# Performance work log

Measured on AMD Instinct MI355X. Metric: run time of the kernel, lower is better.

The kernel has to match this reference:

```python
import jax, jax.numpy as jnp
import numpy as np

IMG_SIZE = 640
STRIDES = (8, 16, 32)
KA = 3          # anchors per level
C = 80          # num classes
CONF_THRESH = 0.001
NMS_THRESH = 0.6
TOPK = 4096     # fixed candidate cap for jit-compatible NMS


def setup_inputs() -> dict:
    key = jax.random.key(0)
    k1, k2, k3 = jax.random.split(key, 3)
    ch = KA * (1 + C + 4)  # 255
    pred_s = jax.random.normal(k1, (ch, 80, 80), dtype=jnp.float32)
    pred_m = jax.random.normal(k2, (ch, 40, 40), dtype=jnp.float32)
    pred_l = jax.random.normal(k3, (ch, 20, 20), dtype=jnp.float32)
    # classic YOLOv3 anchors, [level, anchor, (w,h)]
    anchor_size = jnp.array(
        [[[10, 13], [16, 30], [33, 23]],
         [[30, 61], [62, 45], [59, 119]],
         [[116, 90], [156, 198], [373, 326]]], dtype=jnp.float32)
    return {"pred_s": pred_s, "pred_m": pred_m, "pred_l": pred_l,
            "anchor_size": anchor_size}


def _decode_level(pred, anchors, stride):
    # pred: [KA*(1+C+4), H, W]; anchors: [KA, 2]
    H, W = pred.shape[1], pred.shape[2]
    p = jnp.transpose(pred, (1, 2, 0))                    # [H, W, ch]
    obj = p[..., :KA].reshape(-1, 1)                      # [H*W*KA, 1]
    cls = p[..., KA:KA * (1 + C)].reshape(-1, C)          # [H*W*KA, C]
    reg = p[..., KA * (1 + C):].reshape(H * W, KA, 4)     # [H*W, KA, 4]
    gy, gx = jnp.meshgrid(jnp.arange(H), jnp.arange(W), indexing="ij")
    grid = jnp.stack([gx, gy], -1).reshape(-1, 1, 2).astype(pred.dtype)  # [H*W,1,2]
    # center_sample = False branch
    xy = (jax.nn.sigmoid(reg[..., :2]) + grid) * stride
    wh = jnp.exp(reg[..., 2:]) * anchors[None, :, :]
    box = jnp.concatenate([xy - 0.5 * wh, xy + 0.5 * wh], -1).reshape(-1, 4)
    return obj, cls, box


def _decode(pred_s, pred_m, pred_l, anchor_size):
    parts = [_decode_level(p, anchor_size[i], STRIDES[i])
             for i, p in enumerate([pred_s, pred_m, pred_l])]
    obj = jnp.concatenate([p[0] for p in parts], 0)       # [N,1]
    cls = jnp.concatenate([p[1] for p in parts], 0)       # [N,C]
    box = jnp.concatenate([p[2] for p in parts], 0)       # [N,4]
    bboxes = jnp.clip(box / IMG_SIZE, 0.0, 1.0)
    scores = jax.nn.sigmoid(obj) * jax.nn.softmax(cls, axis=-1)
    return bboxes, scores


def reference(pred_s, pred_m, pred_l, anchor_size):
    bboxes, scores = _decode(pred_s, pred_m, pred_l, anchor_size)
    cls_inds = jnp.argmax(scores, axis=1)                 # [N]
    sc = jnp.max(scores, axis=1)                          # [N]
    sc_masked = jnp.where(sc >= CONF_THRESH, sc, -1.0)
    top_sc, idx = jax.lax.top_k(sc_masked, TOPK)          # candidates, score-sorted
    b = bboxes[idx]                                       # [K,4]
    c = cls_inds[idx]                                     # [K]
    valid = top_sc >= CONF_THRESH                         # [K]
    # pairwise IoU, exactly as the numpy NMS computes it
    x1, y1, x2, y2 = b[:, 0], b[:, 1], b[:, 2], b[:, 3]
    area = (x2 - x1) * (y2 - y1)
    xx1 = jnp.maximum(x1[:, None], x1[None, :])
    yy1 = jnp.maximum(y1[:, None], y1[None, :])
    xx2 = jnp.minimum(x2[:, None], x2[None, :])
    yy2 = jnp.minimum(y2[:, None], y2[None, :])
    w = jnp.maximum(1e-28, xx2 - xx1)
    h = jnp.maximum(1e-28, yy2 - yy1)
    inter = w * h
    iou = inter / (area[:, None] + area[None, :] - inter + 1e-14)
    # sup[j, i] = kept j (earlier in score order) suppresses i, same class only
    order = jnp.arange(TOPK)
    sup = (c[:, None] == c[None, :]) & (iou > NMS_THRESH) \
          & (order[:, None] < order[None, :])
    def body(i, keep):
        ki = valid[i] & ~jnp.any(keep & sup[:, i])
        return keep.at[i].set(ki)
    keep = jax.lax.fori_loop(0, TOPK, body, jnp.zeros(TOPK, dtype=bool))
    return b, top_sc, c, keep
```

## Files before the change

kernel.cpp:

```cpp
#include <hip/hip_runtime.h>
#include <cstdint>
#include <cstddef>

#define N_ANCH 25200
#define NB0 19200
#define NB1 24000
#define TOPK_N 4096
#define CONF_T 0.001
#define NMS_T 0.6
#define IMGS 640.0
#define NBINS 16384
#define JS 16

typedef unsigned long long u64;

struct WS {
  double sc[N_ANCH];
  double box[N_ANCH][4];
  int    cls[N_ANCH];
  int    rank[N_ANCH];
  int    subset[N_ANCH];
  int    hist[NBINS];
  int    m_count;
  int    t_bin;
  double tbox[TOPK_N][4];
  double tarea[TOPK_N];
  double tsc[TOPK_N];
  int    tcls[TOPK_N];
  u64    supT[TOPK_N * 64];
  u64    hasSup[64];
};

__device__ __forceinline__ double dsigmoid(double x) { return 1.0 / (1.0 + exp(-x)); }

__device__ __forceinline__ int score_bin(double sc) {
  if (sc < 0.0) return 0;
  return (int)(__float_as_uint((float)sc) >> 16);
}

__global__ void k_zero(WS* __restrict__ ws) {
  int t = blockIdx.x * 256 + threadIdx.x;
  ws->hist[t] = 0;
  if (t < 64) ws->hasSup[t] = 0ull;
  if (t == 64) ws->m_count = 0;
  if (t == 65) ws->t_bin = 0;
}

__global__ void k_decode(const float* __restrict__ ps, const float* __restrict__ pm,
                         const float* __restrict__ pl, const float* __restrict__ anch,
                         WS* __restrict__ ws) {
  int a = blockIdx.x * 256 + threadIdx.x;
  if (a >= N_ANCH) return;
  const float* p; int W, base, lvl; double stride;
  if (a < NB0)      { p = ps; W = 80; base = 0;   lvl = 0; stride = 8.0; }
  else if (a < NB1) { p = pm; W = 40; base = NB0; lvl = 1; stride = 16.0; }
  else              { p = pl; W = 20; base = NB1; lvl = 2; stride = 32.0; }
  int e = a - base;
  int pos = e / 3;
  int k = e - 3 * pos;
  int HW = W * W;
  int x = pos % W, y = pos / W;

  double sobj = dsigmoid((double)p[(size_t)k * HW + pos]);

  const float* pc = p + (size_t)(3 + k * 80) * HW + pos;
  double m = -1e300, ssum = 0.0; int am = 0;
  for (int c = 0; c < 80; ++c) {
    double v = (double)pc[(size_t)c * HW];
    ssum += exp(v);
    if (v > m) { m = v; am = c; }
  }
  double sc = sobj * (exp(m) / ssum);

  const float* pr = p + (size_t)(243 + k * 4) * HW + pos;
  double tx = (double)pr[0];
  double ty = (double)pr[(size_t)HW];
  double tw = (double)pr[(size_t)2 * HW];
  double th = (double)pr[(size_t)3 * HW];
  double cx = (dsigmoid(tx) + (double)x) * stride;
  double cy = (dsigmoid(ty) + (double)y) * stride;
  double aw = (double)anch[lvl * 6 + k * 2 + 0];
  double ah = (double)anch[lvl * 6 + k * 2 + 1];
  double bw = exp(tw) * aw;
  double bh = exp(th) * ah;
  double x1 = fmin(fmax((cx - 0.5 * bw) / IMGS, 0.0), 1.0);
  double y1 = fmin(fmax((cy - 0.5 * bh) / IMGS, 0.0), 1.0);
  double x2 = fmin(fmax((cx + 0.5 * bw) / IMGS, 0.0), 1.0);
  double y2 = fmin(fmax((cy + 0.5 * bh) / IMGS, 0.0), 1.0);

  ws->box[a][0] = x1; ws->box[a][1] = y1;
  ws->box[a][2] = x2; ws->box[a][3] = y2;
  ws->cls[a] = am;
  double scm = (sc >= CONF_T) ? sc : -1.0;
  ws->sc[a] = scm;
  atomicAdd(&ws->hist[score_bin(scm)], 1);
}

__global__ void k_select(WS* __restrict__ ws) {
  __shared__ int part[256];
  int t = threadIdx.x;
  const int CH = NBINS / 256;
  int sum = 0;
  for (int r = 0; r < CH; ++r) sum += ws->hist[NBINS - 1 - (t * CH + r)];
  part[t] = sum;
  __syncthreads();
  for (int off = 1; off < 256; off <<= 1) {
    int v = (t >= off) ? part[t - off] : 0;
    __syncthreads();
    part[t] += v;
    __syncthreads();
  }
  int exc = part[t] - sum;
  int cum = exc;
  for (int r = 0; r < CH; ++r) {
    int b = NBINS - 1 - (t * CH + r);
    int h = ws->hist[b];
    int prev = cum;
    cum += h;
    if (prev < TOPK_N && cum >= TOPK_N) ws->t_bin = b;
  }
}

__global__ void k_compact(WS* __restrict__ ws) {
  int i = blockIdx.x * 256 + threadIdx.x;
  if (i >= N_ANCH) return;
  int tb = ws->t_bin;
  if (score_bin(ws->sc[i]) >= tb) {
    int idx = atomicAdd(&ws->m_count, 1);
    ws->subset[idx] = i;
    ws->rank[idx] = 0;
  }
}

__global__ void k_rank(WS* __restrict__ ws) {
  const int CHUNK = 1024;
  __shared__ double sj[CHUNK];
  __shared__ int    aj[CHUNK];
  int m = ws->m_count;
  if ((int)blockIdx.x * 256 >= m) return;
  int i = blockIdx.x * 256 + threadIdx.x;
  bool active = (i < m);
  int ai = active ? ws->subset[i] : 0;
  double si = active ? ws->sc[ai] : -2.0;

  int jlen = (m + JS - 1) / JS;
  int j0 = blockIdx.y * jlen;
  int jend = min(j0 + jlen, m);
  int cnt = 0;
  for (int jc = j0; jc < jend; jc += CHUNK) {
    int n = min(CHUNK, jend - jc);
    __syncthreads();
    for (int t = threadIdx.x; t < n; t += 256) {
      int a = ws->subset[jc + t];
      aj[t] = a;
      sj[t] = ws->sc[a];
    }
    __syncthreads();
    if (active) {
      for (int t = 0; t < n; ++t) {
        double s = sj[t];
        cnt += (int)((s > si) | ((s == si) & (aj[t] < ai)));
      }
    }
  }
  if (active && cnt) atomicAdd(&ws->rank[i], cnt);
}

__global__ void k_scatter(WS* __restrict__ ws, float* __restrict__ out) {
  int m = ws->m_count;
  int i = blockIdx.x * 256 + threadIdx.x;
  if (i >= m) return;
  int r = ws->rank[i];
  if (r >= TOPK_N) return;
  int a = ws->subset[i];
  double b0 = ws->box[a][0], b1 = ws->box[a][1];
  double b2 = ws->box[a][2], b3 = ws->box[a][3];
  double s  = ws->sc[a];
  int    c  = ws->cls[a];
  ws->tbox[r][0] = b0; ws->tbox[r][1] = b1;
  ws->tbox[r][2] = b2; ws->tbox[r][3] = b3;
  ws->tarea[r] = (b2 - b0) * (b3 - b1);
  ws->tsc[r] = s;
  ws->tcls[r] = c;
  out[r * 4 + 0] = (float)b0;
  out[r * 4 + 1] = (float)b1;
  out[r * 4 + 2] = (float)b2;
  out[r * 4 + 3] = (float)b3;
  out[4 * TOPK_N + r] = (float)s;
  out[5 * TOPK_N + r] = (float)c;
}

__global__ void k_iou(WS* __restrict__ ws) {
  __shared__ double jb[64][5];
  __shared__ int jc[64];
  int tid = threadIdx.x;
  int w = blockIdx.y;
  if (tid < 64) {
    int j = w * 64 + tid;
    jb[tid][0] = ws->tbox[j][0];
    jb[tid][1] = ws->tbox[j][1];
    jb[tid][2] = ws->tbox[j][2];
    jb[tid][3] = ws->tbox[j][3];
    jb[tid][4] = ws->tarea[j];
    jc[tid] = ws->tcls[j];
  }
  __syncthreads();
  int i = blockIdx.x * 256 + tid;
  double x1 = ws->tbox[i][0], y1 = ws->tbox[i][1];
  double x2 = ws->tbox[i][2], y2 = ws->tbox[i][3];
  double ai = ws->tarea[i];
  int ci = ws->tcls[i];
  u64 bits = 0;
  int jbase = w * 64;
  for (int t = 0; t < 64; ++t) {
    double xx1 = fmax(x1, jb[t][0]);
    double yy1 = fmax(y1, jb[t][1]);
    double xx2 = fmin(x2, jb[t][2]);
    double yy2 = fmin(y2, jb[t][3]);
    double iw = fmax(1e-28, xx2 - xx1);
    double ih = fmax(1e-28, yy2 - yy1);
    double inter = iw * ih;
    double denom = ai + jb[t][4] - inter + 1e-14;
    bool sup = (jc[t] == ci) && (inter > NMS_T * denom) && ((jbase + t) < i);
    bits |= ((u64)sup) << t;
  }
  ws->supT[(size_t)i * 64 + w] = bits;
  if (bits) atomicOr(&ws->hasSup[i >> 6], 1ull << (i & 63));
}

__global__ void __launch_bounds__(64) k_nms(const WS* __restrict__ ws, float* __restrict__ out) {
  __shared__ u64 hsArr[64];
  __shared__ int lst[TOPK_N];
  int lane = threadIdx.x;

  u64 validw = 0;
  for (int b = 0; b < 64; ++b)
    validw |= ((u64)(ws->tsc[lane * 64 + b] >= CONF_T)) << b;

  u64 hasw = ws->hasSup[lane];
  u64 keepw = validw & ~hasw;
  hsArr[lane] = hasw;
  __syncthreads();

  int K = 0;
  for (int l = 0; l < 64; ++l) {
    u64 w = hsArr[l];
    while (w) {
      int b = __builtin_ctzll(w);
      w &= w - 1;
      if (lane == 0) lst[K] = l * 64 + b;
      ++K;
    }
  }
  __syncthreads();

  const u64* ST = ws->supT;
  int IA[16], IB[16];
  u64 A[16], B[16];

#pragma unroll
  for (int r = 0; r < 16; ++r) IA[r] = (r < K) ? lst[r] : 0;
#pragma unroll
  for (int r = 0; r < 16; ++r) A[r] = (r < K) ? ST[(size_t)IA[r] * 64 + lane] : 0ull;

  for (int base = 0; base < K; base += 32) {
#pragma unroll
    for (int r = 0; r < 16; ++r) IB[r] = (base + 16 + r < K) ? lst[base + 16 + r] : 0;
#pragma unroll
    for (int r = 0; r < 16; ++r) B[r] = (base + 16 + r < K) ? ST[(size_t)IB[r] * 64 + lane] : 0ull;
#pragma unroll
    for (int r = 0; r < 16; ++r) {
      if (base + r < K) {
        int i = IA[r];
        u64 bal = __ballot((keepw & A[r]) != 0ull);
        if (lane == (i >> 6) && bal == 0ull && ((validw >> (i & 63)) & 1ull))
          keepw |= 1ull << (i & 63);
      }
    }
#pragma unroll
    for (int r = 0; r < 16; ++r) IA[r] = (base + 32 + r < K) ? lst[base + 32 + r] : 0;
#pragma unroll
    for (int r = 0; r < 16; ++r) A[r] = (base + 32 + r < K) ? ST[(size_t)IA[r] * 64 + lane] : 0ull;
#pragma unroll
    for (int r = 0; r < 16; ++r) {
      if (base + 16 + r < K) {
        int i = IB[r];
        u64 bal = __ballot((keepw & B[r]) != 0ull);
        if (lane == (i >> 6) && bal == 0ull && ((validw >> (i & 63)) & 1ull))
          keepw |= 1ull << (i & 63);
      }
    }
  }

  for (int b = 0; b < 64; ++b)
    out[6 * TOPK_N + lane * 64 + b] = (float)((keepw >> b) & 1ull);
}

extern "C" void kernel_launch(void* const* d_in, const int* in_sizes, int n_in,
                              void* d_out, int out_size, void* d_ws, size_t ws_size,
                              hipStream_t stream) {
  const float* ps   = (const float*)d_in[0];
  const float* pm   = (const float*)d_in[1];
  const float* pl   = (const float*)d_in[2];
  const float* anch = (const float*)d_in[3];
  float* out = (float*)d_out;
  WS* ws = (WS*)d_ws;

  dim3 blk(256);
  k_zero   <<<dim3(NBINS / 256), blk, 0, stream>>>(ws);
  k_decode <<<dim3((N_ANCH + 255) / 256), blk, 0, stream>>>(ps, pm, pl, anch, ws);
  k_select <<<dim3(1), blk, 0, stream>>>(ws);
  k_compact<<<dim3((N_ANCH + 255) / 256), blk, 0, stream>>>(ws);
  k_rank   <<<dim3((N_ANCH + 255) / 256, JS), blk, 0, stream>>>(ws);
  k_scatter<<<dim3((N_ANCH + 255) / 256), blk, 0, stream>>>(ws, out);
  k_iou    <<<dim3(TOPK_N / 256, 64), blk, 0, stream>>>(ws);
  k_nms    <<<dim3(1), dim3(64), 0, stream>>>(ws, out);
}
```

Baseline: 144.3 us.

## Split class softmax across lanes, build histogram in shared memory, skip upper-triangle IoU

```diff
diff --git a/kernel.cpp b/kernel.cpp
--- a/kernel.cpp
+++ b/kernel.cpp
@@ -9,47 +9,42 @@
 #define CONF_T 0.001
 #define NMS_T 0.6
 #define IMGS 640.0
-#define NBINS 16384
+#define NBINS 8192
 #define JS 16
 
 typedef unsigned long long u64;
 
 struct WS {
-  double sc[N_ANCH];
-  double box[N_ANCH][4];
-  int    cls[N_ANCH];
-  int    rank[N_ANCH];
-  int    subset[N_ANCH];
-  int    hist[NBINS];
+  alignas(64) double sc[N_ANCH];
+  alignas(64) double box[N_ANCH][4];
+  alignas(64) int    cls[N_ANCH];
+  alignas(64) int    binv[N_ANCH];
+  alignas(64) int    rank[N_ANCH];
+  alignas(64) int    subset[N_ANCH];
+  alignas(64) double ssc[N_ANCH];
   int    m_count;
   int    t_bin;
-  double tbox[TOPK_N][4];
-  double tarea[TOPK_N];
-  double tsc[TOPK_N];
-  int    tcls[TOPK_N];
-  u64    supT[TOPK_N * 64];
-  u64    hasSup[64];
+  alignas(64) double tbox[TOPK_N][4];
+  alignas(64) double tarea[TOPK_N];
+  alignas(64) double tsc[TOPK_N];
+  alignas(64) int    tcls[TOPK_N];
+  alignas(64) u64    supT[TOPK_N * 64];
+  alignas(64) u64    hasSup[64];
 };
 
 __device__ __forceinline__ double dsigmoid(double x) { return 1.0 / (1.0 + exp(-x)); }
 
 __device__ __forceinline__ int score_bin(double sc) {
   if (sc < 0.0) return 0;
-  return (int)(__float_as_uint((float)sc) >> 16);
-}
-
-__global__ void k_zero(WS* __restrict__ ws) {
-  int t = blockIdx.x * 256 + threadIdx.x;
-  ws->hist[t] = 0;
-  if (t < 64) ws->hasSup[t] = 0ull;
-  if (t == 64) ws->m_count = 0;
-  if (t == 65) ws->t_bin = 0;
+  return (int)(__float_as_uint((float)sc) >> 17);
 }
 
 __global__ void k_decode(const float* __restrict__ ps, const float* __restrict__ pm,
                          const float* __restrict__ pl, const float* __restrict__ anch,
                          WS* __restrict__ ws) {
-  int a = blockIdx.x * 256 + threadIdx.x;
+  int tid = blockIdx.x * 256 + threadIdx.x;
+  int a = tid >> 2;
+  int r = tid & 3;
   if (a >= N_ANCH) return;
   const float* p; int W, base, lvl; double stride;
   if (a < NB0)      { p = ps; W = 80; base = 0;   lvl = 0; stride = 8.0; }
@@ -59,75 +54,92 @@
   int pos = e / 3;
   int k = e - 3 * pos;
   int HW = W * W;
-  int x = pos % W, y = pos / W;
-
-  double sobj = dsigmoid((double)p[(size_t)k * HW + pos]);
 
   const float* pc = p + (size_t)(3 + k * 80) * HW + pos;
   double m = -1e300, ssum = 0.0; int am = 0;
-  for (int c = 0; c < 80; ++c) {
+  for (int t = 0; t < 20; ++t) {
+    int c = r + 4 * t;
     double v = (double)pc[(size_t)c * HW];
     ssum += exp(v);
     if (v > m) { m = v; am = c; }
   }
-  double sc = sobj * (exp(m) / ssum);
-
-  const float* pr = p + (size_t)(243 + k * 4) * HW + pos;
-  double tx = (double)pr[0];
-  double ty = (double)pr[(size_t)HW];
-  double tw = (double)pr[(size_t)2 * HW];
-  double th = (double)pr[(size_t)3 * HW];
-  double cx = (dsigmoid(tx) + (double)x) * stride;
-  double cy = (dsigmoid(ty) + (double)y) * stride;
-  double aw = (double)anch[lvl * 6 + k * 2 + 0];
-  double ah = (double)anch[lvl * 6 + k * 2 + 1];
-  double bw = exp(tw) * aw;
-  double bh = exp(th) * ah;
-  double x1 = fmin(fmax((cx - 0.5 * bw) / IMGS, 0.0), 1.0);
-  double y1 = fmin(fmax((cy - 0.5 * bh) / IMGS, 0.0), 1.0);
-  double x2 = fmin(fmax((cx + 0.5 * bw) / IMGS, 0.0), 1.0);
-  double y2 = fmin(fmax((cy + 0.5 * bh) / IMGS, 0.0), 1.0);
-
-  ws->box[a][0] = x1; ws->box[a][1] = y1;
-  ws->box[a][2] = x2; ws->box[a][3] = y2;
-  ws->cls[a] = am;
-  double scm = (sc >= CONF_T) ? sc : -1.0;
-  ws->sc[a] = scm;
-  atomicAdd(&ws->hist[score_bin(scm)], 1);
-}
-
-__global__ void k_select(WS* __restrict__ ws) {
-  __shared__ int part[256];
+  for (int off = 1; off <= 2; off <<= 1) {
+    double om = __shfl_xor(m, off);
+    int oam   = __shfl_xor(am, off);
+    double os = __shfl_xor(ssum, off);
+    ssum += os;
+    if (om > m || (om == m && oam < am)) { m = om; am = oam; }
+  }
+
+  if (r == 0) {
+    double sobj = dsigmoid((double)p[(size_t)k * HW + pos]);
+    double sc = sobj * (exp(m) / ssum);
+
+    int x = pos % W, y = pos / W;
+    const float* pr = p + (size_t)(243 + k * 4) * HW + pos;
+    double tx = (double)pr[0];
+    double ty = (double)pr[(size_t)HW];
+    double tw = (double)pr[(size_t)2 * HW];
+    double th = (double)pr[(size_t)3 * HW];
+    double cx = (dsigmoid(tx) + (double)x) * stride;
+    double cy = (dsigmoid(ty) + (double)y) * stride;
+    double aw = (double)anch[lvl * 6 + k * 2 + 0];
+    double ah = (double)anch[lvl * 6 + k * 2 + 1];
+    double bw = exp(tw) * aw;
+    double bh = exp(th) * ah;
+    double x1 = fmin(fmax((cx - 0.5 * bw) / IMGS, 0.0), 1.0);
+    double y1 = fmin(fmax((cy - 0.5 * bh) / IMGS, 0.0), 1.0);
+    double x2 = fmin(fmax((cx + 0.5 * bw) / IMGS, 0.0), 1.0);
+    double y2 = fmin(fmax((cy + 0.5 * bh) / IMGS, 0.0), 1.0);
+
+    ws->box[a][0] = x1; ws->box[a][1] = y1;
+    ws->box[a][2] = x2; ws->box[a][3] = y2;
+    ws->cls[a] = am;
+    double scm = (sc >= CONF_T) ? sc : -1.0;
+    ws->sc[a] = scm;
+    ws->binv[a] = score_bin(scm);
+  }
+}
+
+__global__ void __launch_bounds__(1024) k_select(WS* __restrict__ ws) {
+  __shared__ int hist[NBINS];
+  __shared__ int part[1024];
   int t = threadIdx.x;
-  const int CH = NBINS / 256;
+  for (int i = t; i < NBINS; i += 1024) hist[i] = 0;
+  __syncthreads();
+  for (int i = t; i < N_ANCH; i += 1024) atomicAdd(&hist[ws->binv[i]], 1);
+  __syncthreads();
+  const int CH = NBINS / 1024;
   int sum = 0;
-  for (int r = 0; r < CH; ++r) sum += ws->hist[NBINS - 1 - (t * CH + r)];
+  for (int rr = 0; rr < CH; ++rr) sum += hist[NBINS - 1 - (t * CH + rr)];
   part[t] = sum;
   __syncthreads();
-  for (int off = 1; off < 256; off <<= 1) {
+  for (int off = 1; off < 1024; off <<= 1) {
     int v = (t >= off) ? part[t - off] : 0;
     __syncthreads();
     part[t] += v;
     __syncthreads();
   }
-  int exc = part[t] - sum;
-  int cum = exc;
-  for (int r = 0; r < CH; ++r) {
-    int b = NBINS - 1 - (t * CH + r);
-    int h = ws->hist[b];
+  int cum = part[t] - sum;
+  for (int rr = 0; rr < CH; ++rr) {
+    int b = NBINS - 1 - (t * CH + rr);
+    int h = hist[b];
     int prev = cum;
     cum += h;
     if (prev < TOPK_N && cum >= TOPK_N) ws->t_bin = b;
   }
+  if (t == 0) ws->m_count = 0;
 }
 
 __global__ void k_compact(WS* __restrict__ ws) {
   int i = blockIdx.x * 256 + threadIdx.x;
+  if (i < 64) ws->hasSup[i] = 0ull;
   if (i >= N_ANCH) return;
   int tb = ws->t_bin;
-  if (score_bin(ws->sc[i]) >= tb) {
+  if (ws->binv[i] >= tb) {
     int idx = atomicAdd(&ws->m_count, 1);
     ws->subset[idx] = i;
+    ws->ssc[idx] = ws->sc[i];
     ws->rank[idx] = 0;
   }
 }
@@ -141,7 +153,7 @@
   int i = blockIdx.x * 256 + threadIdx.x;
   bool active = (i < m);
   int ai = active ? ws->subset[i] : 0;
-  double si = active ? ws->sc[ai] : -2.0;
+  double si = active ? ws->ssc[i] : -2.0;
 
   int jlen = (m + JS - 1) / JS;
   int j0 = blockIdx.y * jlen;
@@ -151,9 +163,8 @@
     int n = min(CHUNK, jend - jc);
     __syncthreads();
     for (int t = threadIdx.x; t < n; t += 256) {
-      int a = ws->subset[jc + t];
-      aj[t] = a;
-      sj[t] = ws->sc[a];
+      aj[t] = ws->subset[jc + t];
+      sj[t] = ws->ssc[jc + t];
     }
     __syncthreads();
     if (active) {
@@ -175,7 +186,7 @@
   int a = ws->subset[i];
   double b0 = ws->box[a][0], b1 = ws->box[a][1];
   double b2 = ws->box[a][2], b3 = ws->box[a][3];
-  double s  = ws->sc[a];
+  double s  = ws->ssc[i];
   int    c  = ws->cls[a];
   ws->tbox[r][0] = b0; ws->tbox[r][1] = b1;
   ws->tbox[r][2] = b2; ws->tbox[r][3] = b3;
@@ -191,12 +202,18 @@
 }
 
 __global__ void k_iou(WS* __restrict__ ws) {
+  int tid = threadIdx.x;
+  int w = blockIdx.y;
+  int i0 = blockIdx.x * 256;
+  int jbase = w * 64;
+  if (jbase >= i0 + 256) {
+    ws->supT[(size_t)(i0 + tid) * 64 + w] = 0ull;
+    return;
+  }
   __shared__ double jb[64][5];
   __shared__ int jc[64];
-  int tid = threadIdx.x;
-  int w = blockIdx.y;
   if (tid < 64) {
-    int j = w * 64 + tid;
+    int j = jbase + tid;
     jb[tid][0] = ws->tbox[j][0];
     jb[tid][1] = ws->tbox[j][1];
     jb[tid][2] = ws->tbox[j][2];
@@ -205,13 +222,12 @@
     jc[tid] = ws->tcls[j];
   }
   __syncthreads();
-  int i = blockIdx.x * 256 + tid;
+  int i = i0 + tid;
   double x1 = ws->tbox[i][0], y1 = ws->tbox[i][1];
   double x2 = ws->tbox[i][2], y2 = ws->tbox[i][3];
   double ai = ws->tarea[i];
   int ci = ws->tcls[i];
   u64 bits = 0;
-  int jbase = w * 64;
   for (int t = 0; t < 64; ++t) {
     double xx1 = fmax(x1, jb[t][0]);
     double yy1 = fmax(y1, jb[t][1]);
@@ -234,8 +250,14 @@
   int lane = threadIdx.x;
 
   u64 validw = 0;
-  for (int b = 0; b < 64; ++b)
-    validw |= ((u64)(ws->tsc[lane * 64 + b] >= CONF_T)) << b;
+  const double4* tp = (const double4*)(ws->tsc + lane * 64);
+  for (int q = 0; q < 16; ++q) {
+    double4 v = tp[q];
+    validw |= ((u64)(v.x >= CONF_T)) << (q * 4 + 0);
+    validw |= ((u64)(v.y >= CONF_T)) << (q * 4 + 1);
+    validw |= ((u64)(v.z >= CONF_T)) << (q * 4 + 2);
+    validw |= ((u64)(v.w >= CONF_T)) << (q * 4 + 3);
+  }
 
   u64 hasw = ws->hasSup[lane];
   u64 keepw = validw & ~hasw;
@@ -307,9 +329,8 @@
   WS* ws = (WS*)d_ws;
 
   dim3 blk(256);
-  k_zero   <<<dim3(NBINS / 256), blk, 0, stream>>>(ws);
-  k_decode <<<dim3((N_ANCH + 255) / 256), blk, 0, stream>>>(ps, pm, pl, anch, ws);
-  k_select <<<dim3(1), blk, 0, stream>>>(ws);
+  k_decode <<<dim3((N_ANCH * 4 + 255) / 256), blk, 0, stream>>>(ps, pm, pl, anch, ws);
+  k_select <<<dim3(1), dim3(1024), 0, stream>>>(ws);
   k_compact<<<dim3((N_ANCH + 255) / 256), blk, 0, stream>>>(ws);
   k_rank   <<<dim3((N_ANCH + 255) / 256, JS), blk, 0, stream>>>(ws);
   k_scatter<<<dim3((N_ANCH + 255) / 256), blk, 0, stream>>>(ws, out);
```

Result: faster. 123.6 us (-14.4%).
